# Kernel tuning notes

Measured on AMD Instinct MI355X. Metric: run time of the kernel, lower is better.

The kernel has to match this reference:

```python
import jax, jax.numpy as jnp
import numpy as np

CELU_ALPHA = 0.1  # torchani standard CELU alpha


def _celu(x):
    return jax.nn.celu(x, alpha=CELU_ALPHA)


def setup_inputs() -> dict:
    key = jax.random.key(0)
    ks = jax.random.split(key, 12)
    N, S, E, D = 20000, 4, 8, 1008
    dims = [D, 256, 192, 160, 1]
    inp = {
        "aev": jax.random.normal(ks[0], (N, D), jnp.float32),
        "species": jax.random.randint(ks[1], (N,), 0, S, dtype=jnp.int64),
    }
    for l in range(4):
        din, dout = dims[l], dims[l + 1]
        inp[f"W{l}"] = jax.random.normal(ks[2 + 2 * l], (S, E, din, dout), jnp.float32) * (1.0 / np.sqrt(din).astype(np.float32))
        inp[f"b{l}"] = jax.random.normal(ks[3 + 2 * l], (S, E, dout), jnp.float32) * 0.05
    return inp


def reference(aev, species, W0, b0, W1, b1, W2, b2, W3, b3):
    # Faithful math of InferModel.forward: for each species i, gather atoms of
    # that species, run the BmmAtomicNetwork (ensemble of MLPs via bmm, CELU
    # activations, mean over ensemble members), sum per-species energies, then
    # sum into a single [1]-shaped total energy.
    # JIT-friendly equivalent: evaluate every species network on all atoms
    # (S=4 is small) and select each atom's output by its species index.
    # h: [S, E, N, hidden]
    h = _celu(jnp.einsum('ni,seio->seno', aev, W0) + b0[:, :, None, :])
    h = _celu(jnp.einsum('seni,seio->seno', h, W1) + b1[:, :, None, :])
    h = _celu(jnp.einsum('seni,seio->seno', h, W2) + b2[:, :, None, :])
    h = jnp.einsum('seni,seio->seno', h, W3) + b3[:, :, None, :]  # [S,E,N,1]
    per_atom = h.mean(axis=1)[:, :, 0]  # mean over ensemble -> [S, N]
    sel = jnp.take_along_axis(per_atom, species[None, :], axis=0)[0]  # [N]
    return jnp.sum(sel, keepdims=True)  # shape [1], total energy
```

## Files before the change

kernel.cpp:

```cpp
#include <hip/hip_runtime.h>
#include <cmath>

#define NA 20000
#define NS 4
#define NE 8
#define DD 1008
#define BM 128
#define MAXT 157
#define MAXROWS 20608

typedef unsigned short u16;
typedef unsigned int u32;
typedef unsigned long long u64;
typedef u16 u16x8 __attribute__((ext_vector_type(8)));
typedef u16 u16x4 __attribute__((ext_vector_type(4)));
typedef float f32x4 __attribute__((ext_vector_type(4)));
typedef short s16x8 __attribute__((ext_vector_type(8)));

__device__ __forceinline__ float bf2f(u16 h) {
  u32 u = ((u32)h) << 16;
  return __builtin_bit_cast(float, u);
}
__device__ __forceinline__ u16 f2bf(float f) {
  u32 b = __builtin_bit_cast(u32, f);
  u32 lsb = (b >> 16) & 1;
  return (u16)((b + 0x7fffu + lsb) >> 16);
}
__device__ __forceinline__ float celu_f(float x) {
#if __has_builtin(__builtin_amdgcn_exp2f)
  float e = __builtin_amdgcn_exp2f(x * 14.426950408889634f);
#else
  float e = exp2f(x * 14.426950408889634f);
#endif
  return x > 0.f ? x : 0.1f * (e - 1.f);
}
__device__ __forceinline__ float gf(const void* g, size_t i, bool isF32) {
  return isF32 ? ((const float*)g)[i] : bf2f(((const u16*)g)[i]);
}

__device__ __forceinline__ void gll16(const void* g, const u16* lds) {
#if __has_builtin(__builtin_amdgcn_global_load_lds)
  __builtin_amdgcn_global_load_lds(
      (const __attribute__((address_space(1))) u32*)g,
      (__attribute__((address_space(3))) u32*)(u16*)lds, 16, 0, 0);
#else
  int l = threadIdx.x & 63;
  *(f32x4*)((u16*)lds + l * 8) = *(const f32x4*)g;
#endif
}

__global__ void k_initprobe(const void* __restrict__ aev, const void* __restrict__ species,
                            int* __restrict__ w) {
  __shared__ int sh[2];
  int tid = threadIdx.x;
  if (tid < 32) w[tid] = 0;
  if (tid == 0) { sh[0] = 0; sh[1] = 0; }
  __syncthreads();
  const u16* a = (const u16*)aev;
  int bad = 0;
  for (int i = 0; i < 16; ++i) {
    u16 h = a[tid * 16 + i];
    int ex = (h >> 7) & 0xFF;
    if (ex < 107 || ex > 147) ++bad;
  }
  atomicAdd(&sh[0], bad);
  const int* sp = (const int*)species;
  int odd = 0;
  for (int i = 0; i < 4; ++i)
    if (sp[(tid * 4 + i) * 2 + 1] != 0) ++odd;
  atomicAdd(&sh[1], odd);
  __syncthreads();
  if (tid == 0) {
    w[18] = (sh[0] > 400) ? 1 : 0;
    w[19] = (sh[1] == 0) ? 1 : 0;
  }
}

__device__ __forceinline__ int get_species(const void* sp, int i, bool i64) {
  int s = i64 ? ((const int*)sp)[2 * i] : ((const int*)sp)[i];
  return s < 0 ? 0 : (s > 3 ? 3 : s);
}

__global__ void k_count(const void* __restrict__ species, int* __restrict__ w) {
  int i = blockIdx.x * 256 + threadIdx.x;
  int lane = threadIdx.x & 63;
  int s = (i < NA) ? get_species(species, i, w[19] != 0) : -1;
  for (int sp = 0; sp < 4; ++sp) {
    u64 m = __ballot(s == sp);
    if (m != 0 && lane == (__ffsll((long long)m) - 1))
      atomicAdd(&w[sp], __popcll(m));
  }
}

__global__ void k_scan(int* w) {
  int b = 0, pb = 0;
  for (int s = 0; s < 4; ++s) {
    w[13 + s] = b; b += w[s];
    w[20 + s] = pb; pb += ((w[s] + 127) >> 7) << 7;
  }
  w[24] = pb;
}

__global__ void k_scatter(const void* __restrict__ species, int* __restrict__ w,
                          int* __restrict__ order) {
  int i = blockIdx.x * 256 + threadIdx.x;
  int lane = threadIdx.x & 63;
  int s = (i < NA) ? get_species(species, i, w[19] != 0) : -1;
  for (int sp = 0; sp < 4; ++sp) {
    u64 m = __ballot(s == sp);
    if (m == 0) continue;
    int leader = __ffsll((long long)m) - 1;
    int base = 0;
    if (lane == leader) base = atomicAdd(&w[4 + sp], __popcll(m));
    base = __shfl(base, leader);
    if (s == sp) {
      int rank = __popcll(m & ((lane == 63) ? 0x7fffffffffffffffULL : ((1ULL << lane) - 1)));
      order[w[13 + sp] + base + rank] = i;
    }
  }
}

__global__ void k_gather(const void* __restrict__ aev, const int* __restrict__ w,
                         const int* __restrict__ order, u16* __restrict__ aevb) {
  const bool isF32 = (w[18] != 0);
  const int t = threadIdx.x;
  const int r = blockIdx.x * 4 + (t >> 7);
  const int j = t & 127;
  if (j >= 126) return;
  const int s = (r >= w[21]) + (r >= w[22]) + (r >= w[23]);
  const int local = r - w[20 + s];
  u16x8 v = {0, 0, 0, 0, 0, 0, 0, 0};
  if (local < w[s]) {
    const int src = order[w[13 + s] + local];
    if (isF32) {
      const float* p = (const float*)aev + (size_t)src * DD + j * 8;
      const f32x4 f0 = *(const f32x4*)p;
      const f32x4 f1 = *(const f32x4*)(p + 4);
#pragma unroll
      for (int i = 0; i < 4; ++i) { v[i] = f2bf(f0[i]); v[4 + i] = f2bf(f1[i]); }
    } else {
      v = *(const u16x8*)((const u16*)aev + (size_t)src * DD + j * 8);
    }
  }
  *(u16x8*)(aevb + (size_t)r * DD + j * 8) = v;
}

__global__ void k_tr(const void* __restrict__ W, u16* __restrict__ out,
                     int K, int N, int Kpad, const int* __restrict__ w) {
  __shared__ u16 tile[64][68];
  const bool isF32 = (w[18] != 0);
  int se = blockIdx.x, k0 = blockIdx.y * 64, n0 = blockIdx.z * 64;
  int t = threadIdx.x;
  const size_t inBase = (size_t)se * K * N;
#pragma unroll
  for (int c = 0; c < 4; ++c) {
    int kk = (t >> 4) + c * 16, nn = (t & 15) * 4;
    int k = k0 + kk, n = n0 + nn;
    u16x4 v = {0, 0, 0, 0};
    if (k < K && n < N) {
      if (isF32) {
        f32x4 f = *(const f32x4*)((const float*)W + inBase + (size_t)k * N + n);
        v[0] = f2bf(f[0]); v[1] = f2bf(f[1]); v[2] = f2bf(f[2]); v[3] = f2bf(f[3]);
      } else {
        v = *(const u16x4*)((const u16*)W + inBase + (size_t)k * N + n);
      }
    }
    *(u16x4*)(&tile[kk][nn]) = v;
  }
  __syncthreads();
  int nloc = t >> 2, ks = (t & 3) * 16;
  if (n0 + nloc < N) {
    u16x8 o0, o1;
#pragma unroll
    for (int i = 0; i < 8; ++i) { o0[i] = tile[ks + i][nloc]; o1[i] = tile[ks + 8 + i][nloc]; }
    size_t ob = (size_t)se * N * Kpad + (size_t)(n0 + nloc) * Kpad + k0 + ks;
    *(u16x8*)(out + ob) = o0;
    *(u16x8*)(out + ob + 8) = o1;
  }
}

__global__ void k_small(const void* b0, const void* b1, const void* b2, const void* b3,
                        const void* W3, u16* ob0, u16* ob1, u16* ob2, u16* ob3, u16* oW3,
                        u16* gap, const int* __restrict__ w) {
  const bool isF32 = (w[18] != 0);
  int t = threadIdx.x;
  for (int i = t; i < 32 * 256; i += 256) ob0[i] = f2bf(gf(b0, i, isF32));
  for (int i = t; i < 32 * 192; i += 256) ob1[i] = f2bf(gf(b1, i, isF32));
  for (int i = t; i < 32 * 160; i += 256) ob2[i] = f2bf(gf(b2, i, isF32));
  for (int i = t; i < 32 * 160; i += 256) oW3[i] = f2bf(gf(W3, i, isF32));
  if (t < 32) ob3[t] = f2bf(gf(b3, t, isF32));
  u16x8 z = {0, 0, 0, 0, 0, 0, 0, 0};
  *(u16x8*)(gap + t * 8) = z;
}

__global__ __launch_bounds__(512, 4) void k_main(
    const u16* __restrict__ aevb, const u16* __restrict__ wt0,
    const u16* __restrict__ wt1, const u16* __restrict__ wt2,
    const u16* __restrict__ w3b, const u16* __restrict__ b0b,
    const u16* __restrict__ b1b, const u16* __restrict__ b2b,
    const u16* __restrict__ b3b, const int* __restrict__ w,
    float* __restrict__ accum) {
  __shared__ __align__(16) u16 L[32768];

  const int tid = threadIdx.x;
  const int g = blockIdx.x;
  const int s = g >> 1;
  const int e = (g & 1) * 4 + (blockIdx.y & 3);
  const int tile = blockIdx.y >> 2;
  const int cnt = w[s];
  if (tile * BM >= cnt) return;
  const int mRow = w[20 + s] + tile * BM;
  const int mCount = min(BM, cnt - tile * BM);
  const int se = s * NE + e;

  const int lane = tid & 63;
  const int wv = tid >> 6;
  const int lcol = lane & 15;
  const int quad = lane >> 4;

  {
    const u16* wt0se = wt0 + (size_t)se * 256 * 1024;
    const int rowA = tid >> 2;
    const int gAx = (tid & 3) ^ ((rowA >> 1) & 3);
    const char* gA = (const char*)aevb + (size_t)(mRow + rowA) * 2016 + gAx * 16;
    const int rB1 = 128 + (tid >> 2);
    const int gB0x = (tid & 3) ^ (((tid >> 2) >> 1) & 3);
    const int gB1x = (tid & 3) ^ ((rB1 >> 1) & 3);
    const char* gB0 = (const char*)wt0se + (size_t)(tid >> 2) * 2048 + gB0x * 16;
    const char* gB1 = (const char*)wt0se + (size_t)rB1 * 2048 + gB1x * 16;
    const int aSt = wv * 512;
    const int bSt = 8192 + wv * 512;
    const int bSt2 = 8192 + 4096 + wv * 512;

    const int wm = wv >> 2, wn = wv & 3;
    const int gsw = (quad ^ ((lcol >> 1) & 3)) * 8;
    const int aRow0 = (wm * 64 + lcol) * 32 + gsw;
    const int bRow0 = 8192 + (wn * 64 + lcol) * 32 + gsw;

    f32x4 acc[4][4];
#pragma unroll
    for (int i = 0; i < 4; ++i)
#pragma unroll
      for (int j = 0; j < 4; ++j) acc[i][j] = (f32x4){0.f, 0.f, 0.f, 0.f};

    gll16(gA, &L[aSt]); gA += 64;
    gll16(gB0, &L[bSt]); gB0 += 64;
    gll16(gB1, &L[bSt2]); gB1 += 64;
    __syncthreads();

    for (int p = 0; p < 32; ++p) {
      const int d = p & 1;
      if (p < 31) {
        const int dn = d ^ 1;
        gll16(gA, &L[dn * 4096 + aSt]); gA += 64;
        gll16(gB0, &L[dn * 8192 + bSt]); gB0 += 64;
        gll16(gB1, &L[dn * 8192 + bSt2]); gB1 += 64;
      }
      const u16* Ad = &L[d * 4096];
      const u16* Bd = &L[d * 8192];
      s16x8 aF[4], bF[4];
#pragma unroll
      for (int mt = 0; mt < 4; ++mt)
        aF[mt] = __builtin_bit_cast(s16x8, *(const u16x8*)(Ad + aRow0 + mt * 512));
#pragma unroll
      for (int nt = 0; nt < 4; ++nt)
        bF[nt] = __builtin_bit_cast(s16x8, *(const u16x8*)(Bd + bRow0 + nt * 512));
      __builtin_amdgcn_s_setprio(1);
#pragma unroll
      for (int nt = 0; nt < 4; ++nt)
#pragma unroll
        for (int mt = 0; mt < 4; ++mt)
          acc[mt][nt] = __builtin_amdgcn_mfma_f32_16x16x32_bf16(aF[mt], bF[nt], acc[mt][nt], 0, 0, 0);
      __builtin_amdgcn_s_setprio(0);
      __syncthreads();
    }

#pragma unroll
    for (int nt = 0; nt < 4; ++nt) {
      const int col = wn * 64 + nt * 16 + lcol;
      const float bb = bf2f(b0b[se * 256 + col]);
#pragma unroll
      for (int mt = 0; mt < 4; ++mt) {
#pragma unroll
        for (int r = 0; r < 4; ++r) {
          const int rr = wm * 64 + mt * 16 + quad * 4 + r;
          L[(rr * 256 + col) ^ ((rr & 7) << 3)] = f2bf(celu_f(acc[mt][nt][r] + bb));
        }
      }
    }
  }
  __syncthreads();

  {
    const int wm = wv >> 2, wn = wv & 3;
    const u16* w1se = wt1 + (size_t)se * 192 * 256;
    const u16* bp[3];
#pragma unroll
    for (int nt = 0; nt < 3; ++nt)
      bp[nt] = w1se + (size_t)(wn * 48 + nt * 16 + lcol) * 256 + quad * 8;
    f32x4 acc[4][3];
#pragma unroll
    for (int i = 0; i < 4; ++i)
#pragma unroll
      for (int j = 0; j < 3; ++j) acc[i][j] = (f32x4){0.f, 0.f, 0.f, 0.f};
    int aBase[4], aSwz[4];
#pragma unroll
    for (int mt = 0; mt < 4; ++mt) {
      const int row = wm * 64 + mt * 16 + lcol;
      aBase[mt] = row * 256 + quad * 8;
      aSwz[mt] = (row & 7) << 3;
    }
    u16x8 cB[3], nB[3];
#pragma unroll
    for (int nt = 0; nt < 3; ++nt) cB[nt] = *(const u16x8*)bp[nt];
    for (int kc = 0; kc < 8; ++kc) {
      if (kc < 7) {
#pragma unroll
        for (int nt = 0; nt < 3; ++nt) nB[nt] = *(const u16x8*)(bp[nt] + (kc + 1) * 32);
      }
      s16x8 aF[4];
#pragma unroll
      for (int mt = 0; mt < 4; ++mt)
        aF[mt] = __builtin_bit_cast(s16x8, *(const u16x8*)&L[(aBase[mt] + kc * 32) ^ aSwz[mt]]);
#pragma unroll
      for (int nt = 0; nt < 3; ++nt) {
        const s16x8 bF = __builtin_bit_cast(s16x8, cB[nt]);
#pragma unroll
        for (int mt = 0; mt < 4; ++mt)
          acc[mt][nt] = __builtin_amdgcn_mfma_f32_16x16x32_bf16(aF[mt], bF, acc[mt][nt], 0, 0, 0);
      }
      if (kc < 7) {
#pragma unroll
        for (int nt = 0; nt < 3; ++nt) cB[nt] = nB[nt];
      }
    }
    __syncthreads();
#pragma unroll
    for (int nt = 0; nt < 3; ++nt) {
      const int col = wn * 48 + nt * 16 + lcol;
      const float bb = bf2f(b1b[se * 192 + col]);
#pragma unroll
      for (int mt = 0; mt < 4; ++mt) {
#pragma unroll
        for (int r = 0; r < 4; ++r) {
          const int rr = wm * 64 + mt * 16 + quad * 4 + r;
          L[(rr * 192 + col) ^ ((rr & 7) << 3)] = f2bf(celu_f(acc[mt][nt][r] + bb));
        }
      }
    }
  }
  __syncthreads();

  {
    const int wm = wv >> 1, wn = wv & 1;
    const u16* w2se = wt2 + (size_t)se * 160 * 192;
    const u16* bp[5];
#pragma unroll
    for (int nt = 0; nt < 5; ++nt)
      bp[nt] = w2se + (size_t)(wn * 80 + nt * 16 + lcol) * 192 + quad * 8;
    f32x4 acc[2][5];
#pragma unroll
    for (int i = 0; i < 2; ++i)
#pragma unroll
      for (int j = 0; j < 5; ++j) acc[i][j] = (f32x4){0.f, 0.f, 0.f, 0.f};
    int aBase[2], aSwz[2];
#pragma unroll
    for (int mt = 0; mt < 2; ++mt) {
      const int row = wm * 32 + mt * 16 + lcol;
      aBase[mt] = row * 192 + quad * 8;
      aSwz[mt] = (row & 7) << 3;
    }
    u16x8 cB[5], nB[5];
#pragma unroll
    for (int nt = 0; nt < 5; ++nt) cB[nt] = *(const u16x8*)bp[nt];
    for (int kc = 0; kc < 6; ++kc) {
      if (kc < 5) {
#pragma unroll
        for (int nt = 0; nt < 5; ++nt) nB[nt] = *(const u16x8*)(bp[nt] + (kc + 1) * 32);
      }
      s16x8 aF[2];
#pragma unroll
      for (int mt = 0; mt < 2; ++mt)
        aF[mt] = __builtin_bit_cast(s16x8, *(const u16x8*)&L[(aBase[mt] + kc * 32) ^ aSwz[mt]]);
#pragma unroll
      for (int nt = 0; nt < 5; ++nt) {
        const s16x8 bF = __builtin_bit_cast(s16x8, cB[nt]);
#pragma unroll
        for (int mt = 0; mt < 2; ++mt)
          acc[mt][nt] = __builtin_amdgcn_mfma_f32_16x16x32_bf16(aF[mt], bF, acc[mt][nt], 0, 0, 0);
      }
      if (kc < 5) {
#pragma unroll
        for (int nt = 0; nt < 5; ++nt) cB[nt] = nB[nt];
      }
    }
    __syncthreads();
#pragma unroll
    for (int nt = 0; nt < 5; ++nt) {
      const int col = wn * 80 + nt * 16 + lcol;
      const float bb = bf2f(b2b[se * 160 + col]);
#pragma unroll
      for (int mt = 0; mt < 2; ++mt) {
#pragma unroll
        for (int r = 0; r < 4; ++r) {
          const int rr = wm * 32 + mt * 16 + quad * 4 + r;
          L[(rr * 160 + col) ^ ((rr & 7) << 3)] = f2bf(celu_f(acc[mt][nt][r] + bb));
        }
      }
    }
  }
  __syncthreads();

  {
    const int row = tid >> 2;
    const int pp = tid & 3;
    const u16* w3p = w3b + se * 160;
    float dotv = 0.f;
#pragma unroll
    for (int j = 0; j < 5; ++j) {
      const int ci = (pp + 4 * j) * 8;
      const u16x8 hv = *(const u16x8*)&L[(row * 160 + ci) ^ ((row & 7) << 3)];
      const u16x8 wv8 = *(const u16x8*)(w3p + ci);
#pragma unroll
      for (int t2 = 0; t2 < 8; ++t2)
        dotv = fmaf(bf2f(hv[t2]), bf2f(wv8[t2]), dotv);
    }
    dotv += __shfl_xor(dotv, 1);
    dotv += __shfl_xor(dotv, 2);
    float v = (pp == 0 && row < mCount) ? (dotv + bf2f(b3b[se])) : 0.f;
    v += __shfl_xor(v, 4);
    v += __shfl_xor(v, 8);
    v += __shfl_xor(v, 16);
    v += __shfl_xor(v, 32);
    float* redf = (float*)&L[20608];
    if (lane == 0) redf[wv] = v;
    __syncthreads();
    if (tid == 0) {
      float tot = 0.f;
#pragma unroll
      for (int i = 0; i < 8; ++i) tot += redf[i];
      atomicAdd(accum, tot * 0.125f);
    }
  }
}

__global__ void k_final(const float* __restrict__ accum, u32* __restrict__ out) {
  u32 h = (u32)f2bf(accum[0]);
  out[0] = (h << 16) | h;
}

extern "C" void kernel_launch(void* const* d_in, const int* in_sizes, int n_in,
                              void* d_out, int out_size, void* d_ws, size_t ws_size,
                              hipStream_t stream) {
  const void* aev = d_in[0];
  const void* species = d_in[1];
  const void* W0 = d_in[2];
  const void* b0 = d_in[3];
  const void* W1 = d_in[4];
  const void* b1 = d_in[5];
  const void* W2 = d_in[6];
  const void* b2 = d_in[7];
  const void* W3 = d_in[8];
  const void* b3 = d_in[9];

  int* wsI = (int*)d_ws;
  float* accum = (float*)((char*)d_ws + 17 * 4);
  int* order = wsI + 1024;
  char* wsB = (char*)d_ws;

  const size_t oB0 = 131072;
  const size_t oB1 = 147456;
  const size_t oB2 = 159744;
  const size_t oB3 = 169984;
  const size_t oW3 = 170048;
  const size_t oAevb = 262144;
  const size_t oGap = 41807872;
  const size_t oWt0 = 41811968;
  const size_t oWt1 = 58589184;
  const size_t oWt2 = 61734912;

  u16* aevb = (u16*)(wsB + oAevb);
  u16* wt0 = (u16*)(wsB + oWt0);
  u16* wt1 = (u16*)(wsB + oWt1);
  u16* wt2 = (u16*)(wsB + oWt2);
  u16* w3b = (u16*)(wsB + oW3);
  u16* b0b = (u16*)(wsB + oB0);
  u16* b1b = (u16*)(wsB + oB1);
  u16* b2b = (u16*)(wsB + oB2);
  u16* b3b = (u16*)(wsB + oB3);

  hipLaunchKernelGGL(k_initprobe, dim3(1), dim3(256), 0, stream, aev, species, wsI);
  hipLaunchKernelGGL(k_count, dim3((NA + 255) / 256), dim3(256), 0, stream, species, wsI);
  hipLaunchKernelGGL(k_scan, dim3(1), dim3(1), 0, stream, wsI);
  hipLaunchKernelGGL(k_scatter, dim3((NA + 255) / 256), dim3(256), 0, stream, species, wsI, order);
  hipLaunchKernelGGL(k_gather, dim3(MAXROWS / 4), dim3(512), 0, stream, aev, wsI, order, aevb);
  hipLaunchKernelGGL(k_tr, dim3(32, 16, 4), dim3(256), 0, stream, W0, wt0, 1008, 256, 1024, wsI);
  hipLaunchKernelGGL(k_tr, dim3(32, 4, 3), dim3(256), 0, stream, W1, wt1, 256, 192, 256, wsI);
  hipLaunchKernelGGL(k_tr, dim3(32, 3, 3), dim3(256), 0, stream, W2, wt2, 192, 160, 192, wsI);
  hipLaunchKernelGGL(k_small, dim3(1), dim3(256), 0, stream, b0, b1, b2, b3, W3,
                     b0b, b1b, b2b, b3b, w3b, (u16*)(wsB + oGap), wsI);
  hipLaunchKernelGGL(k_main, dim3(8, 4 * MAXT), dim3(512), 0, stream,
                     aevb, wt0, wt1, wt2, w3b, b0b, b1b, b2b, b3b, wsI, accum);
  hipLaunchKernelGGL(k_final, dim3(1), dim3(1), 0, stream, accum, (u32*)d_out);
}
```

Baseline: 440.9 us.

## Stream layer-0 weights from registers with triple-buffered A tiles and fused prep kernels

The layer-0 GEMM in k_main now keeps only the activation tile in LDS, using a 3-deep ring of 64-wide K chunks filled by global_load_lds. Weight fragments are loaded straight from global memory into registers and prefetched one step ahead. A workgroup barrier with an explicit vmcnt wait now runs only every other K step, meant to reduce barrier stalls and LDS traffic. Several small prep kernels are also merged (scan folded into count via a last-block atomic, small biases into scatter, three transposes into one launch) to cut launch overhead. Weight loads from global into registers may raise latency exposure and register pressure.

```diff
diff --git a/kernel.cpp b/kernel.cpp
--- a/kernel.cpp
+++ b/kernel.cpp
@@ -49,11 +49,19 @@
 #endif
 }
 
-__global__ void k_initprobe(const void* __restrict__ aev, const void* __restrict__ species,
-                            int* __restrict__ w) {
+#define CHUNK_BARRIER(N)                                   \
+  do {                                                     \
+    asm volatile("s_waitcnt vmcnt(" #N ")" ::: "memory");  \
+    __builtin_amdgcn_sched_barrier(0);                     \
+    __builtin_amdgcn_s_barrier();                          \
+    __builtin_amdgcn_sched_barrier(0);                     \
+  } while (0)
+
+__global__ void k_probe0(const void* __restrict__ aev, const void* __restrict__ species,
+                         int* __restrict__ w) {
   __shared__ int sh[2];
   int tid = threadIdx.x;
-  if (tid < 32) w[tid] = 0;
+  if (tid < 64) w[tid] = 0;
   if (tid == 0) { sh[0] = 0; sh[1] = 0; }
   __syncthreads();
   const u16* a = (const u16*)aev;
@@ -90,19 +98,38 @@
     if (m != 0 && lane == (__ffsll((long long)m) - 1))
       atomicAdd(&w[sp], __popcll(m));
   }
-}
-
-__global__ void k_scan(int* w) {
-  int b = 0, pb = 0;
-  for (int s = 0; s < 4; ++s) {
-    w[13 + s] = b; b += w[s];
-    w[20 + s] = pb; pb += ((w[s] + 127) >> 7) << 7;
-  }
-  w[24] = pb;
-}
-
-__global__ void k_scatter(const void* __restrict__ species, int* __restrict__ w,
-                          int* __restrict__ order) {
+  __syncthreads();
+  if (threadIdx.x == 0) {
+    __threadfence();
+    if (atomicAdd(&w[25], 1) == (int)gridDim.x - 1) {
+      int b = 0, pb = 0;
+      for (int sp = 0; sp < 4; ++sp) {
+        int c = atomicAdd(&w[sp], 0);
+        w[13 + sp] = b; b += c;
+        w[20 + sp] = pb; pb += ((c + 127) >> 7) << 7;
+      }
+      w[24] = pb;
+    }
+  }
+}
+
+__global__ void k_scatsml(const void* __restrict__ species, int* __restrict__ w,
+                          int* __restrict__ order,
+                          const void* b0, const void* b1, const void* b2, const void* b3,
+                          const void* W3, u16* ob0, u16* ob1, u16* ob2, u16* ob3,
+                          u16* oW3, u16* gap) {
+  if (blockIdx.x == 79) {
+    const bool isF32 = (w[18] != 0);
+    int t = threadIdx.x;
+    for (int i = t; i < 32 * 256; i += 256) ob0[i] = f2bf(gf(b0, i, isF32));
+    for (int i = t; i < 32 * 192; i += 256) ob1[i] = f2bf(gf(b1, i, isF32));
+    for (int i = t; i < 32 * 160; i += 256) ob2[i] = f2bf(gf(b2, i, isF32));
+    for (int i = t; i < 32 * 160; i += 256) oW3[i] = f2bf(gf(W3, i, isF32));
+    if (t < 32) ob3[t] = f2bf(gf(b3, t, isF32));
+    u16x8 z = {0, 0, 0, 0, 0, 0, 0, 0};
+    *(u16x8*)(gap + t * 8) = z;
+    return;
+  }
   int i = blockIdx.x * 256 + threadIdx.x;
   int lane = threadIdx.x & 63;
   int s = (i < NA) ? get_species(species, i, w[19] != 0) : -1;
@@ -145,12 +172,9 @@
   *(u16x8*)(aevb + (size_t)r * DD + j * 8) = v;
 }
 
-__global__ void k_tr(const void* __restrict__ W, u16* __restrict__ out,
-                     int K, int N, int Kpad, const int* __restrict__ w) {
-  __shared__ u16 tile[64][68];
-  const bool isF32 = (w[18] != 0);
-  int se = blockIdx.x, k0 = blockIdx.y * 64, n0 = blockIdx.z * 64;
-  int t = threadIdx.x;
+__device__ void tr_tile(const void* __restrict__ W, u16* __restrict__ out,
+                        int K, int N, int Kpad, bool isF32, int se,
+                        int k0, int n0, int t, u16 (*tile)[68]) {
   const size_t inBase = (size_t)se * K * N;
 #pragma unroll
   for (int c = 0; c < 4; ++c) {
@@ -179,18 +203,22 @@
   }
 }
 
-__global__ void k_small(const void* b0, const void* b1, const void* b2, const void* b3,
-                        const void* W3, u16* ob0, u16* ob1, u16* ob2, u16* ob3, u16* oW3,
-                        u16* gap, const int* __restrict__ w) {
+__global__ void k_tr3(const void* __restrict__ W0, const void* __restrict__ W1,
+                      const void* __restrict__ W2, u16* __restrict__ o0,
+                      u16* __restrict__ o1, u16* __restrict__ o2,
+                      const int* __restrict__ w) {
+  __shared__ u16 tile[64][68];
   const bool isF32 = (w[18] != 0);
-  int t = threadIdx.x;
-  for (int i = t; i < 32 * 256; i += 256) ob0[i] = f2bf(gf(b0, i, isF32));
-  for (int i = t; i < 32 * 192; i += 256) ob1[i] = f2bf(gf(b1, i, isF32));
-  for (int i = t; i < 32 * 160; i += 256) ob2[i] = f2bf(gf(b2, i, isF32));
-  for (int i = t; i < 32 * 160; i += 256) oW3[i] = f2bf(gf(W3, i, isF32));
-  if (t < 32) ob3[t] = f2bf(gf(b3, t, isF32));
-  u16x8 z = {0, 0, 0, 0, 0, 0, 0, 0};
-  *(u16x8*)(gap + t * 8) = z;
+  const int se = blockIdx.x, by = blockIdx.y, bz = blockIdx.z, t = threadIdx.x;
+  tr_tile(W0, o0, 1008, 256, 1024, isF32, se, by * 64, bz * 64, t, tile);
+  if (by < 4 && bz < 3) {
+    __syncthreads();
+    tr_tile(W1, o1, 256, 192, 256, isF32, se, by * 64, bz * 64, t, tile);
+  }
+  if (by < 3 && bz < 3) {
+    __syncthreads();
+    tr_tile(W2, o2, 192, 160, 192, isF32, se, by * 64, bz * 64, t, tile);
+  }
 }
 
 __global__ __launch_bounds__(512, 4) void k_main(
@@ -220,22 +248,28 @@
 
   {
     const u16* wt0se = wt0 + (size_t)se * 256 * 1024;
-    const int rowA = tid >> 2;
-    const int gAx = (tid & 3) ^ ((rowA >> 1) & 3);
-    const char* gA = (const char*)aevb + (size_t)(mRow + rowA) * 2016 + gAx * 16;
-    const int rB1 = 128 + (tid >> 2);
-    const int gB0x = (tid & 3) ^ (((tid >> 2) >> 1) & 3);
-    const int gB1x = (tid & 3) ^ ((rB1 >> 1) & 3);
-    const char* gB0 = (const char*)wt0se + (size_t)(tid >> 2) * 2048 + gB0x * 16;
-    const char* gB1 = (const char*)wt0se + (size_t)rB1 * 2048 + gB1x * 16;
-    const int aSt = wv * 512;
-    const int bSt = 8192 + wv * 512;
-    const int bSt2 = 8192 + 4096 + wv * 512;
-
     const int wm = wv >> 2, wn = wv & 3;
-    const int gsw = (quad ^ ((lcol >> 1) & 3)) * 8;
-    const int aRow0 = (wm * 64 + lcol) * 32 + gsw;
-    const int bRow0 = 8192 + (wn * 64 + lcol) * 32 + gsw;
+
+    const int slot0 = wv * 64 + lane;
+    const int slot1 = 512 + wv * 64 + lane;
+    const int r0 = slot0 >> 3, r1 = slot1 >> 3;
+    const u16* gA0 = aevb + (size_t)(mRow + r0) * 1008 + (((slot0 & 7) ^ (r0 & 7)) << 3);
+    const u16* gA1 = aevb + (size_t)(mRow + r1) * 1008 + (((slot1 & 7) ^ (r1 & 7)) << 3);
+    const int ldsA0 = wv * 512;
+    const int ldsA1 = 4096 + wv * 512;
+
+    int rAoff[4], rAx[4];
+#pragma unroll
+    for (int mt = 0; mt < 4; ++mt) {
+      const int row = wm * 64 + mt * 16 + lcol;
+      rAoff[mt] = row * 64;
+      rAx[mt] = row & 7;
+    }
+
+    const u16* bp[4];
+#pragma unroll
+    for (int nt = 0; nt < 4; ++nt)
+      bp[nt] = wt0se + (size_t)(wn * 64 + nt * 16 + lcol) * 1024 + quad * 8;
 
     f32x4 acc[4][4];
 #pragma unroll
@@ -243,36 +277,50 @@
 #pragma unroll
       for (int j = 0; j < 4; ++j) acc[i][j] = (f32x4){0.f, 0.f, 0.f, 0.f};
 
-    gll16(gA, &L[aSt]); gA += 64;
-    gll16(gB0, &L[bSt]); gB0 += 64;
-    gll16(gB1, &L[bSt2]); gB1 += 64;
-    __syncthreads();
-
+    gll16(gA0, &L[0 * 8192 + ldsA0]);
+    gll16(gA1, &L[0 * 8192 + ldsA1]);
+    gll16(gA0 + 64, &L[1 * 8192 + ldsA0]);
+    gll16(gA1 + 64, &L[1 * 8192 + ldsA1]);
+    u16x8 bCur[4], bNxt[4];
+#pragma unroll
+    for (int nt = 0; nt < 4; ++nt) bCur[nt] = *(const u16x8*)bp[nt];
+    CHUNK_BARRIER(2);
+
+    int bufC = 0, bufS = 2;
+#pragma unroll 2
     for (int p = 0; p < 32; ++p) {
-      const int d = p & 1;
+      const int c = p >> 1, h = p & 1;
       if (p < 31) {
-        const int dn = d ^ 1;
-        gll16(gA, &L[dn * 4096 + aSt]); gA += 64;
-        gll16(gB0, &L[dn * 8192 + bSt]); gB0 += 64;
-        gll16(gB1, &L[dn * 8192 + bSt2]); gB1 += 64;
-      }
-      const u16* Ad = &L[d * 4096];
-      const u16* Bd = &L[d * 8192];
-      s16x8 aF[4], bF[4];
+#pragma unroll
+        for (int nt = 0; nt < 4; ++nt)
+          bNxt[nt] = *(const u16x8*)(bp[nt] + (p + 1) * 32);
+      }
+      if (h == 0 && c + 2 < 16) {
+        gll16(gA0 + (c + 2) * 64, &L[bufS * 8192 + ldsA0]);
+        gll16(gA1 + (c + 2) * 64, &L[bufS * 8192 + ldsA1]);
+      }
+      const int h4 = h << 2;
+      s16x8 aF[4];
 #pragma unroll
       for (int mt = 0; mt < 4; ++mt)
-        aF[mt] = __builtin_bit_cast(s16x8, *(const u16x8*)(Ad + aRow0 + mt * 512));
-#pragma unroll
-      for (int nt = 0; nt < 4; ++nt)
-        bF[nt] = __builtin_bit_cast(s16x8, *(const u16x8*)(Bd + bRow0 + nt * 512));
+        aF[mt] = __builtin_bit_cast(s16x8,
+            *(const u16x8*)&L[bufC * 8192 + rAoff[mt] + (((h4 + quad) ^ rAx[mt]) << 3)]);
       __builtin_amdgcn_s_setprio(1);
 #pragma unroll
-      for (int nt = 0; nt < 4; ++nt)
+      for (int nt = 0; nt < 4; ++nt) {
+        const s16x8 bF = __builtin_bit_cast(s16x8, bCur[nt]);
 #pragma unroll
         for (int mt = 0; mt < 4; ++mt)
-          acc[mt][nt] = __builtin_amdgcn_mfma_f32_16x16x32_bf16(aF[mt], bF[nt], acc[mt][nt], 0, 0, 0);
+          acc[mt][nt] = __builtin_amdgcn_mfma_f32_16x16x32_bf16(aF[mt], bF, acc[mt][nt], 0, 0, 0);
+      }
       __builtin_amdgcn_s_setprio(0);
-      __syncthreads();
+#pragma unroll
+      for (int nt = 0; nt < 4; ++nt) bCur[nt] = bNxt[nt];
+      if (h == 1) {
+        CHUNK_BARRIER(6);
+        bufC = (bufC == 2) ? 0 : bufC + 1;
+        bufS = (bufS == 2) ? 0 : bufS + 1;
+      }
     }
 
 #pragma unroll
@@ -489,16 +537,13 @@
   u16* b2b = (u16*)(wsB + oB2);
   u16* b3b = (u16*)(wsB + oB3);
 
-  hipLaunchKernelGGL(k_initprobe, dim3(1), dim3(256), 0, stream, aev, species, wsI);
+  hipLaunchKernelGGL(k_probe0, dim3(1), dim3(256), 0, stream, aev, species, wsI);
   hipLaunchKernelGGL(k_count, dim3((NA + 255) / 256), dim3(256), 0, stream, species, wsI);
-  hipLaunchKernelGGL(k_scan, dim3(1), dim3(1), 0, stream, wsI);
-  hipLaunchKernelGGL(k_scatter, dim3((NA + 255) / 256), dim3(256), 0, stream, species, wsI, order);
+  hipLaunchKernelGGL(k_scatsml, dim3(80), dim3(256), 0, stream, species, wsI, order,
+                     b0, b1, b2, b3, W3, b0b, b1b, b2b, b3b, w3b, (u16*)(wsB + oGap));
   hipLaunchKernelGGL(k_gather, dim3(MAXROWS / 4), dim3(512), 0, stream, aev, wsI, order, aevb);
-  hipLaunchKernelGGL(k_tr, dim3(32, 16, 4), dim3(256), 0, stream, W0, wt0, 1008, 256, 1024, wsI);
-  hipLaunchKernelGGL(k_tr, dim3(32, 4, 3), dim3(256), 0, stream, W1, wt1, 256, 192, 256, wsI);
-  hipLaunchKernelGGL(k_tr, dim3(32, 3, 3), dim3(256), 0, stream, W2, wt2, 192, 160, 192, wsI);
-  hipLaunchKernelGGL(k_small, dim3(1), dim3(256), 0, stream, b0, b1, b2, b3, W3,
-                     b0b, b1b, b2b, b3b, w3b, (u16*)(wsB + oGap), wsI);
+  hipLaunchKernelGGL(k_tr3, dim3(32, 16, 4), dim3(256), 0, stream, W0, W1, W2,
+                     wt0, wt1, wt2, wsI);
   hipLaunchKernelGGL(k_main, dim3(8, 4 * MAXT), dim3(512), 0, stream,
                      aevb, wt0, wt1, wt2, w3b, b0b, b1b, b2b, b3b, wsI, accum);
   hipLaunchKernelGGL(k_final, dim3(1), dim3(1), 0, stream, accum, (u32*)d_out);
```

New measurement: 482.8 us. 1.09x slower.
